# Kernel optimization log

Measured on AMD Instinct MI355X. Metric: run time of the kernel, lower is better.

Reference implementation:

```python
import jax, jax.numpy as jnp
import numpy as np

B = 1024
INPUT_SIZE = 2048
OUTPUT_SIZE = 2048
E = 131072  # number of sparse connections


def setup_inputs() -> dict:
    key = jax.random.key(0)
    k1, k2, k3, k4 = jax.random.split(key, 4)
    x = jax.random.normal(k1, (B, INPUT_SIZE), dtype=jnp.float32)
    weights = jax.random.normal(k2, (E,), dtype=jnp.float32)
    in_idx = jax.random.randint(k3, (E,), 0, INPUT_SIZE, dtype=jnp.int64)
    out_idx = jax.random.randint(k4, (E,), 0, OUTPUT_SIZE, dtype=jnp.int64)
    return {"x": x, "weights": weights, "in_idx": in_idx, "out_idx": out_idx}


def reference(x, weights, in_idx, out_idx):
    # Original: for (i, o), w in connections: output[:, o] += w * x[:, i]
    # Vectorized as a single gather-multiply-scatter (duplicates sum):
    contrib = x[:, in_idx] * weights[None, :]  # [B, E]
    out = jnp.zeros((x.shape[0], OUTPUT_SIZE), dtype=x.dtype)
    out = out.at[:, out_idx].add(contrib)  # scatter-add along output dim
    return out
```

## Files before the change

### kernel.cpp

```cpp
#include <hip/hip_runtime.h>

#define BATCH  1024
#define IN_SZ  2048
#define OUT_SZ 2048
#define E_N    131072

#define NT     256
#define KMAX   128
#define CH     8
#define CPAD   16
#define FBLK   128
#define TBLK   512
#define PBASE  0xAAAAAAAAu

__device__ __forceinline__ unsigned int bf16_rne(float f) {
    unsigned int u = __float_as_uint(f);
    return (u + 0x7FFFu + ((u >> 16) & 1u)) >> 16;
}

__global__ __launch_bounds__(NT) void prep_kernel(
    const float* __restrict__ x,
    const int4* __restrict__ iidx4, const int4* __restrict__ oidx4,
    const float4* __restrict__ w4,
    unsigned short* __restrict__ xt, int* __restrict__ cursor,
    unsigned int* __restrict__ ell) {
    const int tid = threadIdx.x;
    const int b   = blockIdx.x;

    if (b < FBLK) {
        const int q = b * NT + tid;
        const int4   ii = iidx4[q];
        const int4   oo = oidx4[q];
        const float4 ww = w4[q];
        #pragma unroll
        for (int j = 0; j < 4; ++j) {
            const int i = (&ii.x)[j];
            const int o = (&oo.x)[j];
            const unsigned int packed = (bf16_rne((&ww.x)[j]) << 16) | (unsigned int)i;
            const int raw = atomicAdd(&cursor[o * CPAD], 1);
            const unsigned int kp = (unsigned int)raw - PBASE;
            const unsigned int slot = kp < KMAX ? kp : (unsigned int)raw;
            if (slot < KMAX)
                ell[(size_t)o * KMAX + slot] = packed;
        }
    } else {
        __shared__ float lds[64][65];
        const int bt = b - FBLK;
        const int jj = bt & 7, kk = bt >> 3;
        const int r0 = ((((jj >> 2) << 3) | (kk & 7))) * 64;
        const int c0 = ((((kk >> 3) << 2) | (jj & 3))) * 64;
        #pragma unroll
        for (int k = 0; k < 16; ++k) {
            const int idx = k * NT + tid;
            lds[idx >> 6][idx & 63] =
                x[(size_t)(r0 + (idx >> 6)) * IN_SZ + c0 + (idx & 63)];
        }
        __syncthreads();
        #pragma unroll
        for (int k = 0; k < 8; ++k) {
            const int idx = k * NT + tid;
            const int cl = idx >> 5;
            const int rp = (idx & 31) * 2;
            const unsigned int v =
                bf16_rne(lds[rp][cl]) | (bf16_rne(lds[rp + 1][cl]) << 16);
            *(unsigned int*)&xt[(size_t)(c0 + cl) * BATCH + r0 + rp] = v;
        }
    }
}

__global__ __launch_bounds__(NT) void spmm7_kernel(
    const unsigned short* __restrict__ xt, const unsigned int* __restrict__ ell,
    const int* __restrict__ cursor, float* __restrict__ out) {
    __shared__ float tile[4][260];
    const int tid  = threadIdx.x;
    const int wv_  = tid >> 6;
    const int lane = tid & 63;
    const int b    = blockIdx.x;
    const int e    = b & 7;
    const int t    = b >> 3;
    const int r0   = (e >> 1) << 8;
    const int c0   = ((e & 1) << 10) | (t << 2);
    const int cs   = __builtin_amdgcn_readfirstlane(c0 + wv_);

    const int raw = cursor[cs * CPAD];
    const unsigned int ud = (unsigned int)raw - PBASE;
    int cnt = (ud < 256u) ? (int)ud : raw;
    cnt = cnt < 0 ? 0 : (cnt > KMAX ? KMAX : cnt);
    const int nch = (cnt + CH - 1) / CH;
    const unsigned int* ep = ell + (size_t)cs * KMAX;
    const unsigned short* xtb = xt + r0 + lane * 4;

    float a[4];
    #pragma unroll
    for (int k = 0; k < 4; ++k) a[k] = 0.f;

    if (nch > 0) {
        unsigned int e0[CH], e1[CH];
        #pragma unroll
        for (int j = 0; j < CH; ++j) e0[j] = ep[j];
        for (int g = 0; g < nch; ++g) {
            const int gn = (g + 1 < nch) ? g + 1 : g;
            #pragma unroll
            for (int j = 0; j < CH; ++j) e1[j] = ep[gn * CH + j];
            uint2 xv[CH];
            #pragma unroll
            for (int j = 0; j < CH; ++j)
                xv[j] = *(const uint2*)(xtb + ((size_t)(e0[j] & 0x7FFu) << 10));
            #pragma unroll
            for (int j = 0; j < CH; ++j) {
                const float wv = __uint_as_float(e0[j] & 0xFFFF0000u);
                a[0] = fmaf(wv, __uint_as_float(xv[j].x << 16),         a[0]);
                a[1] = fmaf(wv, __uint_as_float(xv[j].x & 0xFFFF0000u), a[1]);
                a[2] = fmaf(wv, __uint_as_float(xv[j].y << 16),         a[2]);
                a[3] = fmaf(wv, __uint_as_float(xv[j].y & 0xFFFF0000u), a[3]);
            }
            #pragma unroll
            for (int j = 0; j < CH; ++j) e0[j] = e1[j];
        }
    }

    *(float4*)&tile[wv_][lane * 4] = make_float4(a[0], a[1], a[2], a[3]);
    __syncthreads();

    {
        const int row = tid;
        float* op = out + (size_t)(r0 + row) * OUT_SZ + c0;
        *(float4*)op = make_float4(tile[0][row], tile[1][row],
                                   tile[2][row], tile[3][row]);
    }
}

__global__ __launch_bounds__(NT) void sparse_row_kernel(
    const float* __restrict__ x, const float* __restrict__ w,
    const int* __restrict__ iidx, const int* __restrict__ oidx,
    float* __restrict__ out) {
    __shared__ float xs[IN_SZ];
    __shared__ float acc[OUT_SZ];
    const int b = blockIdx.x, tid = threadIdx.x;
    const float4* xrow = (const float4*)(x + (size_t)b * IN_SZ);
    float4* xs4 = (float4*)xs;
    for (int t = tid; t < IN_SZ / 4; t += NT) xs4[t] = xrow[t];
    float4* acc4 = (float4*)acc;
    const float4 z = make_float4(0.f, 0.f, 0.f, 0.f);
    for (int t = tid; t < OUT_SZ / 4; t += NT) acc4[t] = z;
    __syncthreads();
    for (int e = tid; e < E_N; e += NT)
        atomicAdd(&acc[oidx[e]], w[e] * xs[iidx[e]]);
    __syncthreads();
    float4* orow = (float4*)(out + (size_t)b * OUT_SZ);
    for (int t = tid; t < OUT_SZ / 4; t += NT) orow[t] = acc4[t];
}

extern "C" void kernel_launch(void* const* d_in, const int* in_sizes, int n_in,
                              void* d_out, int out_size, void* d_ws, size_t ws_size,
                              hipStream_t stream) {
    const float* x    = (const float*)d_in[0];
    const float* wts  = (const float*)d_in[1];
    const int*   iidx = (const int*)d_in[2];
    const int*   oidx = (const int*)d_in[3];
    float* out = (float*)d_out;
    (void)in_sizes; (void)n_in; (void)out_size;

    const size_t cursor_bytes = (size_t)OUT_SZ * CPAD * sizeof(int);
    const size_t ell_bytes    = (size_t)OUT_SZ * KMAX * sizeof(unsigned int);
    const size_t xt_bytes     = (size_t)IN_SZ * BATCH * sizeof(unsigned short);
    if (ws_size < cursor_bytes + ell_bytes + xt_bytes) {
        sparse_row_kernel<<<BATCH, NT, 0, stream>>>(x, wts, iidx, oidx, out);
        return;
    }

    int* cursor = (int*)d_ws;
    unsigned int*   ell = (unsigned int*)((char*)d_ws + cursor_bytes);
    unsigned short* xt  = (unsigned short*)((char*)d_ws + cursor_bytes + ell_bytes);

    prep_kernel<<<FBLK + TBLK, NT, 0, stream>>>(x, (const int4*)iidx,
                                                (const int4*)oidx, (const float4*)wts,
                                                xt, cursor, ell);
    spmm7_kernel<<<2048, NT, 0, stream>>>(xt, ell, cursor, out);
}
```

Before: 93.86 us.

## Split batch into halves, widen per-lane loads, split edge list across wave pairs

The transposed bf16 x buffer is now laid out in two batch halves of 512 rows, so each lane loads 16 bytes (8 batch values) per edge instead of 8. Each block now covers 2 output columns × 512 batch rows, and two waves per column process alternating edge chunks. Their partial sums are combined through shared memory. The software prefetch of ELL entries is removed and CH drops to 4. The intent is wider, better-coalesced gathers and more parallelism per column. In exchange the kernel adds an extra LDS reduction and barrier and narrows the output stores to float2.

```diff
diff --git a/kernel.cpp b/kernel.cpp
--- a/kernel.cpp
+++ b/kernel.cpp
@@ -7,11 +7,12 @@
 
 #define NT     256
 #define KMAX   128
-#define CH     8
+#define CH     4
 #define CPAD   16
 #define FBLK   128
 #define TBLK   512
 #define PBASE  0xAAAAAAAAu
+#define HSH    (IN_SZ * 512)
 
 __device__ __forceinline__ unsigned int bf16_rne(float f) {
     unsigned int u = __float_as_uint(f);
@@ -49,6 +50,8 @@
         const int jj = bt & 7, kk = bt >> 3;
         const int r0 = ((((jj >> 2) << 3) | (kk & 7))) * 64;
         const int c0 = ((((kk >> 3) << 2) | (jj & 3))) * 64;
+        const int h   = r0 >> 9;
+        const int rr0 = r0 & 511;
         #pragma unroll
         for (int k = 0; k < 16; ++k) {
             const int idx = k * NT + tid;
@@ -63,24 +66,28 @@
             const int rp = (idx & 31) * 2;
             const unsigned int v =
                 bf16_rne(lds[rp][cl]) | (bf16_rne(lds[rp + 1][cl]) << 16);
-            *(unsigned int*)&xt[(size_t)(c0 + cl) * BATCH + r0 + rp] = v;
+            *(unsigned int*)&xt[(size_t)h * HSH + (size_t)(c0 + cl) * 512 + rr0 + rp] = v;
         }
     }
 }
 
-__global__ __launch_bounds__(NT) void spmm7_kernel(
+__global__ __launch_bounds__(NT, 8) void spmm9_kernel(
     const unsigned short* __restrict__ xt, const unsigned int* __restrict__ ell,
     const int* __restrict__ cursor, float* __restrict__ out) {
-    __shared__ float tile[4][260];
+    __shared__ float tile[2][516];
+    __shared__ float comb[2][516];
     const int tid  = threadIdx.x;
-    const int wv_  = tid >> 6;
+    const int w    = tid >> 6;
     const int lane = tid & 63;
     const int b    = blockIdx.x;
     const int e    = b & 7;
-    const int t    = b >> 3;
-    const int r0   = (e >> 1) << 8;
-    const int c0   = ((e & 1) << 10) | (t << 2);
-    const int cs   = __builtin_amdgcn_readfirstlane(c0 + wv_);
+    const int u    = b >> 3;
+    const int h    = e >> 2;
+    const int r0   = h << 9;
+    const int c0   = ((e & 3) << 9) | (u << 1);
+    const int col  = c0 + (w & 1);
+    const int eh   = w >> 1;
+    const int cs   = __builtin_amdgcn_readfirstlane(col);
 
     const int raw = cursor[cs * CPAD];
     const unsigned int ud = (unsigned int)raw - PBASE;
@@ -88,45 +95,53 @@
     cnt = cnt < 0 ? 0 : (cnt > KMAX ? KMAX : cnt);
     const int nch = (cnt + CH - 1) / CH;
     const unsigned int* ep = ell + (size_t)cs * KMAX;
-    const unsigned short* xtb = xt + r0 + lane * 4;
+    const unsigned short* xtb = xt + (size_t)h * HSH + lane * 8;
 
-    float a[4];
+    float a[8];
     #pragma unroll
-    for (int k = 0; k < 4; ++k) a[k] = 0.f;
+    for (int k = 0; k < 8; ++k) a[k] = 0.f;
 
-    if (nch > 0) {
-        unsigned int e0[CH], e1[CH];
+    for (int g = eh; g < nch; g += 2) {
+        const int base = g * CH;
+        unsigned int ee[CH];
         #pragma unroll
-        for (int j = 0; j < CH; ++j) e0[j] = ep[j];
-        for (int g = 0; g < nch; ++g) {
-            const int gn = (g + 1 < nch) ? g + 1 : g;
-            #pragma unroll
-            for (int j = 0; j < CH; ++j) e1[j] = ep[gn * CH + j];
-            uint2 xv[CH];
-            #pragma unroll
-            for (int j = 0; j < CH; ++j)
-                xv[j] = *(const uint2*)(xtb + ((size_t)(e0[j] & 0x7FFu) << 10));
-            #pragma unroll
-            for (int j = 0; j < CH; ++j) {
-                const float wv = __uint_as_float(e0[j] & 0xFFFF0000u);
-                a[0] = fmaf(wv, __uint_as_float(xv[j].x << 16),         a[0]);
-                a[1] = fmaf(wv, __uint_as_float(xv[j].x & 0xFFFF0000u), a[1]);
-                a[2] = fmaf(wv, __uint_as_float(xv[j].y << 16),         a[2]);
-                a[3] = fmaf(wv, __uint_as_float(xv[j].y & 0xFFFF0000u), a[3]);
-            }
-            #pragma unroll
-            for (int j = 0; j < CH; ++j) e0[j] = e1[j];
+        for (int j2 = 0; j2 < CH; ++j2) ee[j2] = ep[base + j2];
+        uint4 xv[CH];
+        #pragma unroll
+        for (int j2 = 0; j2 < CH; ++j2)
+            xv[j2] = *(const uint4*)(xtb + ((size_t)(ee[j2] & 0x7FFu) << 9));
+        #pragma unroll
+        for (int j2 = 0; j2 < CH; ++j2) {
+            const float wv = __uint_as_float(ee[j2] & 0xFFFF0000u);
+            a[0] = fmaf(wv, __uint_as_float(xv[j2].x << 16),         a[0]);
+            a[1] = fmaf(wv, __uint_as_float(xv[j2].x & 0xFFFF0000u), a[1]);
+            a[2] = fmaf(wv, __uint_as_float(xv[j2].y << 16),         a[2]);
+            a[3] = fmaf(wv, __uint_as_float(xv[j2].y & 0xFFFF0000u), a[3]);
+            a[4] = fmaf(wv, __uint_as_float(xv[j2].z << 16),         a[4]);
+            a[5] = fmaf(wv, __uint_as_float(xv[j2].z & 0xFFFF0000u), a[5]);
+            a[6] = fmaf(wv, __uint_as_float(xv[j2].w << 16),         a[6]);
+            a[7] = fmaf(wv, __uint_as_float(xv[j2].w & 0xFFFF0000u), a[7]);
         }
     }
 
-    *(float4*)&tile[wv_][lane * 4] = make_float4(a[0], a[1], a[2], a[3]);
+    if (eh) {
+        *(float4*)&comb[w & 1][lane * 8]     = make_float4(a[0], a[1], a[2], a[3]);
+        *(float4*)&comb[w & 1][lane * 8 + 4] = make_float4(a[4], a[5], a[6], a[7]);
+    }
+    __syncthreads();
+    if (!eh) {
+        #pragma unroll
+        for (int k = 0; k < 8; ++k) a[k] += comb[w & 1][lane * 8 + k];
+        *(float4*)&tile[w & 1][lane * 8]     = make_float4(a[0], a[1], a[2], a[3]);
+        *(float4*)&tile[w & 1][lane * 8 + 4] = make_float4(a[4], a[5], a[6], a[7]);
+    }
     __syncthreads();
 
-    {
-        const int row = tid;
+    #pragma unroll
+    for (int rr = 0; rr < 2; ++rr) {
+        const int row = rr * NT + tid;
         float* op = out + (size_t)(r0 + row) * OUT_SZ + c0;
-        *(float4*)op = make_float4(tile[0][row], tile[1][row],
-                                   tile[2][row], tile[3][row]);
+        *(float2*)op = make_float2(tile[0][row], tile[1][row]);
     }
 }
 
@@ -176,5 +191,5 @@
     prep_kernel<<<FBLK + TBLK, NT, 0, stream>>>(x, (const int4*)iidx,
                                                 (const int4*)oidx, (const float4*)wts,
                                                 xt, cursor, ell);
-    spmm7_kernel<<<2048, NT, 0, stream>>>(xt, ell, cursor, out);
+    spmm9_kernel<<<2048, NT, 0, stream>>>(xt, ell, cursor, out);
 }
```

Result: faster. 90.76 us (-3.3%).

## Stage 8-row bf16 x tile in LDS and give one output column per thread

Applied to the files above, without the earlier changes.

The SpMM kernel is restructured so that each block loads an 8-row batch tile of bf16 x for all 2048 inputs into shared memory, padded with stride 5. Each thread then owns one output column and walks its ELL entries, which are now stored transposed (slot-major) so that neighbouring threads read consecutive entries. x is now laid out in 8-row batch blocks. The intent is to replace scattered global gathers with LDS gathers. The cost is about 40KB of LDS per block, possible bank conflicts and divergence across threads with different counts, and scalar output stores.

```diff
diff --git a/kernel.cpp b/kernel.cpp
--- a/kernel.cpp
+++ b/kernel.cpp
@@ -7,11 +7,13 @@
 
 #define NT     256
 #define KMAX   128
-#define CH     8
 #define CPAD   16
 #define FBLK   128
 #define TBLK   512
 #define PBASE  0xAAAAAAAAu
+#define RT     8
+#define NBT    (BATCH / RT)
+#define FSTR   5
 
 __device__ __forceinline__ unsigned int bf16_rne(float f) {
     unsigned int u = __float_as_uint(f);
@@ -22,8 +24,8 @@
     const float* __restrict__ x,
     const int4* __restrict__ iidx4, const int4* __restrict__ oidx4,
     const float4* __restrict__ w4,
-    unsigned short* __restrict__ xt, int* __restrict__ cursor,
-    unsigned int* __restrict__ ell) {
+    unsigned int* __restrict__ xt32, int* __restrict__ cursor,
+    unsigned int* __restrict__ ellT) {
     const int tid = threadIdx.x;
     const int b   = blockIdx.x;
 
@@ -41,7 +43,7 @@
             const unsigned int kp = (unsigned int)raw - PBASE;
             const unsigned int slot = kp < KMAX ? kp : (unsigned int)raw;
             if (slot < KMAX)
-                ell[(size_t)o * KMAX + slot] = packed;
+                ellT[(size_t)slot * OUT_SZ + o] = packed;
         }
     } else {
         __shared__ float lds[64][65];
@@ -63,71 +65,73 @@
             const int rp = (idx & 31) * 2;
             const unsigned int v =
                 bf16_rne(lds[rp][cl]) | (bf16_rne(lds[rp + 1][cl]) << 16);
-            *(unsigned int*)&xt[(size_t)(c0 + cl) * BATCH + r0 + rp] = v;
+            const int bt8  = (r0 + rp) >> 3;
+            const int roff = (r0 + rp) & 7;
+            xt32[(size_t)bt8 * (IN_SZ * RT / 2) + (c0 + cl) * (RT / 2) + (roff >> 1)] = v;
         }
     }
 }
 
-__global__ __launch_bounds__(NT) void spmm7_kernel(
-    const unsigned short* __restrict__ xt, const unsigned int* __restrict__ ell,
+__global__ __launch_bounds__(NT, 4) void spmm12_kernel(
+    const unsigned int* __restrict__ xt32, const unsigned int* __restrict__ ellT,
     const int* __restrict__ cursor, float* __restrict__ out) {
-    __shared__ float tile[4][260];
-    const int tid  = threadIdx.x;
-    const int wv_  = tid >> 6;
-    const int lane = tid & 63;
-    const int b    = blockIdx.x;
-    const int e    = b & 7;
-    const int t    = b >> 3;
-    const int r0   = (e >> 1) << 8;
-    const int c0   = ((e & 1) << 10) | (t << 2);
-    const int cs   = __builtin_amdgcn_readfirstlane(c0 + wv_);
+    __shared__ unsigned int xl[IN_SZ * FSTR];
+    const int tid = threadIdx.x;
+    const int b   = blockIdx.x;
+    const int e   = b & 7;
+    const int s   = b >> 3;
+    const int ti  = s & 15;
+    const int cg  = s >> 4;
+    const int bt  = ti * 8 + e;
+    const int r0  = bt * RT;
+    const int col = (cg << 8) + tid;
 
-    const int raw = cursor[cs * CPAD];
+    const unsigned int* xg = xt32 + (size_t)bt * (IN_SZ * RT / 2);
+    #pragma unroll
+    for (int j = 0; j < 16; ++j) {
+        const int g2 = j * NT + tid;
+        const uint2 v = *(const uint2*)(xg + g2 * 2);
+        const int f = g2 >> 1, hh = (g2 & 1) * 2;
+        xl[f * FSTR + hh]     = v.x;
+        xl[f * FSTR + hh + 1] = v.y;
+    }
+
+    const int raw = cursor[col * CPAD];
     const unsigned int ud = (unsigned int)raw - PBASE;
     int cnt = (ud < 256u) ? (int)ud : raw;
     cnt = cnt < 0 ? 0 : (cnt > KMAX ? KMAX : cnt);
-    const int nch = (cnt + CH - 1) / CH;
-    const unsigned int* ep = ell + (size_t)cs * KMAX;
-    const unsigned short* xtb = xt + r0 + lane * 4;
 
-    float a[4];
+    __syncthreads();
+
+    float a[RT];
     #pragma unroll
-    for (int k = 0; k < 4; ++k) a[k] = 0.f;
+    for (int k = 0; k < RT; ++k) a[k] = 0.f;
 
-    if (nch > 0) {
-        unsigned int e0[CH], e1[CH];
-        #pragma unroll
-        for (int j = 0; j < CH; ++j) e0[j] = ep[j];
-        for (int g = 0; g < nch; ++g) {
-            const int gn = (g + 1 < nch) ? g + 1 : g;
-            #pragma unroll
-            for (int j = 0; j < CH; ++j) e1[j] = ep[gn * CH + j];
-            uint2 xv[CH];
-            #pragma unroll
-            for (int j = 0; j < CH; ++j)
-                xv[j] = *(const uint2*)(xtb + ((size_t)(e0[j] & 0x7FFu) << 10));
-            #pragma unroll
-            for (int j = 0; j < CH; ++j) {
-                const float wv = __uint_as_float(e0[j] & 0xFFFF0000u);
-                a[0] = fmaf(wv, __uint_as_float(xv[j].x << 16),         a[0]);
-                a[1] = fmaf(wv, __uint_as_float(xv[j].x & 0xFFFF0000u), a[1]);
-                a[2] = fmaf(wv, __uint_as_float(xv[j].y << 16),         a[2]);
-                a[3] = fmaf(wv, __uint_as_float(xv[j].y & 0xFFFF0000u), a[3]);
-            }
-            #pragma unroll
-            for (int j = 0; j < CH; ++j) e0[j] = e1[j];
-        }
+    const unsigned int* ep = ellT + col;
+    unsigned int e0 = cnt > 0 ? ep[0] : 0;
+    unsigned int e1 = cnt > 1 ? ep[OUT_SZ] : 0;
+    for (int k = 0; k < cnt; ++k) {
+        const unsigned int en = (k + 2 < cnt) ? ep[(size_t)(k + 2) * OUT_SZ] : 0;
+        const int i = e0 & 0x7FFu;
+        const float wv = __uint_as_float(e0 & 0xFFFF0000u);
+        const unsigned int q0 = xl[i * FSTR + 0];
+        const unsigned int q1 = xl[i * FSTR + 1];
+        const unsigned int q2 = xl[i * FSTR + 2];
+        const unsigned int q3 = xl[i * FSTR + 3];
+        a[0] = fmaf(wv, __uint_as_float(q0 << 16),         a[0]);
+        a[1] = fmaf(wv, __uint_as_float(q0 & 0xFFFF0000u), a[1]);
+        a[2] = fmaf(wv, __uint_as_float(q1 << 16),         a[2]);
+        a[3] = fmaf(wv, __uint_as_float(q1 & 0xFFFF0000u), a[3]);
+        a[4] = fmaf(wv, __uint_as_float(q2 << 16),         a[4]);
+        a[5] = fmaf(wv, __uint_as_float(q2 & 0xFFFF0000u), a[5]);
+        a[6] = fmaf(wv, __uint_as_float(q3 << 16),         a[6]);
+        a[7] = fmaf(wv, __uint_as_float(q3 & 0xFFFF0000u), a[7]);
+        e0 = e1; e1 = en;
     }
 
-    *(float4*)&tile[wv_][lane * 4] = make_float4(a[0], a[1], a[2], a[3]);
-    __syncthreads();
-
-    {
-        const int row = tid;
-        float* op = out + (size_t)(r0 + row) * OUT_SZ + c0;
-        *(float4*)op = make_float4(tile[0][row], tile[1][row],
-                                   tile[2][row], tile[3][row]);
-    }
+    #pragma unroll
+    for (int r = 0; r < RT; ++r)
+        out[(size_t)(r0 + r) * OUT_SZ + col] = a[r];
 }
 
 __global__ __launch_bounds__(NT) void sparse_row_kernel(
@@ -162,7 +166,7 @@
     (void)in_sizes; (void)n_in; (void)out_size;
 
     const size_t cursor_bytes = (size_t)OUT_SZ * CPAD * sizeof(int);
-    const size_t ell_bytes    = (size_t)OUT_SZ * KMAX * sizeof(unsigned int);
+    const size_t ell_bytes    = (size_t)KMAX * OUT_SZ * sizeof(unsigned int);
     const size_t xt_bytes     = (size_t)IN_SZ * BATCH * sizeof(unsigned short);
     if (ws_size < cursor_bytes + ell_bytes + xt_bytes) {
         sparse_row_kernel<<<BATCH, NT, 0, stream>>>(x, wts, iidx, oidx, out);
@@ -170,11 +174,11 @@
     }
 
     int* cursor = (int*)d_ws;
-    unsigned int*   ell = (unsigned int*)((char*)d_ws + cursor_bytes);
-    unsigned short* xt  = (unsigned short*)((char*)d_ws + cursor_bytes + ell_bytes);
+    unsigned int* ellT = (unsigned int*)((char*)d_ws + cursor_bytes);
+    unsigned int* xt32 = (unsigned int*)((char*)d_ws + cursor_bytes + ell_bytes);
 
     prep_kernel<<<FBLK + TBLK, NT, 0, stream>>>(x, (const int4*)iidx,
                                                 (const int4*)oidx, (const float4*)wts,
-                                                xt, cursor, ell);
-    spmm7_kernel<<<2048, NT, 0, stream>>>(xt, ell, cursor, out);
+                                                xt32, cursor, ellT);
+    spmm12_kernel<<<1024, NT, 0, stream>>>(xt32, ellT, cursor, out);
 }
```

New measurement: 96.73 us. +3.1%, slower.
